# Performance work log

Measured on AMD Instinct MI355X. Metric: run time of the kernel, lower is better.

The kernel has to match this reference:

```python
import jax, jax.numpy as jnp
import numpy as np

B, T, F_IN, F_OUT = 16, 2048, 128, 128
ALPHA = 0.2  # LeakyReLU negative slope
MASK_VAL = -1e9


def setup_inputs() -> dict:
    key = jax.random.key(0)
    kx, kw, ka, kadj = jax.random.split(key, 4)
    # xavier_uniform-ish scale for W and a (gain=1.414)
    w_bound = 1.414 * np.sqrt(6.0 / (F_IN + F_OUT))
    a_bound = 1.414 * np.sqrt(6.0 / (2 * F_OUT + 1))
    x = jax.random.normal(kx, (B, T, F_IN), jnp.float32)
    W = jax.random.uniform(kw, (F_IN, F_OUT), jnp.float32, -w_bound, w_bound)
    a = jax.random.uniform(ka, (2 * F_OUT, 1), jnp.float32, -a_bound, a_bound)
    adj = jax.random.randint(kadj, (B, T, T), 0, 2, jnp.int32)
    return {"x": x, "adj": adj, "W": W, "a": a}


def reference(x, adj, W, a):
    # h: [B,T,F_OUT]
    h = jnp.einsum('btf,fo->bto', x, W)
    # Additive GAT score decomposition: e[b,i,j] = leakyrelu(h_i . a1 + h_j . a2)
    # Mathematically identical to cat([h_i,h_j]) @ a, without the BxTxTx2F tensor.
    a1 = a[:F_OUT, 0]   # [F_OUT]
    a2 = a[F_OUT:, 0]   # [F_OUT]
    s1 = h @ a1         # [B,T]
    s2 = h @ a2         # [B,T]
    e = jax.nn.leaky_relu(s1[:, :, None] + s2[:, None, :], ALPHA)  # [B,T,T]
    e = jnp.where(adj == 0, MASK_VAL, e)
    att = jax.nn.softmax(e, axis=-1)  # [B,T,T]
    # dropout=0.0 / eval mode -> identity
    return att @ h  # [B,T,F_OUT]
```

## Files before the change

### kernel.cpp

```cpp
#include <hip/hip_runtime.h>
#include <hip/hip_bf16.h>

#define TT 2048
#define NB 16
#define FD 128
#define ALPHA 0.2f

typedef __attribute__((ext_vector_type(8))) short short8;
typedef __attribute__((ext_vector_type(4))) float f32x4;
typedef __attribute__((ext_vector_type(16))) float f32x16;

static __device__ __forceinline__ unsigned short f2bf(float f) {
    unsigned u = __float_as_uint(f);
    u += 0x7FFF + ((u >> 16) & 1);
    return (unsigned short)(u >> 16);
}
static __device__ __forceinline__ unsigned short bfbits(float f) {
    return __builtin_bit_cast(unsigned short, __float2bfloat16(f));
}

__global__ __launch_bounds__(256) void k_pack(const int* __restrict__ adj,
                                              unsigned char* __restrict__ bm)
{
    const int tid = threadIdx.x;
    const int w = tid >> 6, l = tid & 63;
    const int row = blockIdx.x * 4 + w;
    const int* ap = adj + (size_t)row * TT + l * 4;
    unsigned char* op = bm + (size_t)row * 256;

    #pragma unroll
    for (int rd = 0; rd < 8; ++rd) {
        int4 q = *reinterpret_cast<const int4*>(ap + rd * 256);
        unsigned n =  min((unsigned)q.x, 1u)
                   | (min((unsigned)q.y, 1u) << 1)
                   | (min((unsigned)q.z, 1u) << 2)
                   | (min((unsigned)q.w, 1u) << 3);
        unsigned pn = (unsigned)__shfl_xor((int)n, 1);
        if ((l & 1) == 0)
            op[rd * 32 + (l >> 1)] = (unsigned char)(n | (pn << 4));
    }
}

__global__ __launch_bounds__(256) void k_wt(const float* __restrict__ W,
                                            unsigned short* __restrict__ WT)
{
    int fid = blockIdx.x * 256 + threadIdx.x;
    int k = fid >> 5;
    int f = (fid & 31) << 2;
    float4 w4 = *reinterpret_cast<const float4*>(W + k * FD + f);
    WT[(f + 0) * FD + k] = f2bf(w4.x);
    WT[(f + 1) * FD + k] = f2bf(w4.y);
    WT[(f + 2) * FD + k] = f2bf(w4.z);
    WT[(f + 3) * FD + k] = f2bf(w4.w);
}

__global__ __launch_bounds__(256) void k_h(const float* __restrict__ x,
                                           const unsigned short* __restrict__ WT,
                                           const float* __restrict__ a,
                                           unsigned short* __restrict__ hF,
                                           float* __restrict__ s1,
                                           float* __restrict__ s2)
{
    __shared__ unsigned short hs[128][72];

    const int tid = threadIdx.x;
    const int b  = blockIdx.x >> 5;
    const int t0 = (blockIdx.x & 31) << 6;
    const int w = tid >> 6, l = tid & 63, g = l >> 4, r15 = l & 15;

    const float* xrow = x + ((size_t)(b * TT + t0 + w * 16 + r15)) * FD;

    f32x4 acc[8] = {};

    #pragma unroll
    for (int m = 0; m < 4; ++m) {
        const int koff = m * 32 + g * 8;
        float4 xa = *reinterpret_cast<const float4*>(xrow + koff);
        float4 xb = *reinterpret_cast<const float4*>(xrow + koff + 4);
        short8 af;
        af[0] = (short)f2bf(xa.x); af[1] = (short)f2bf(xa.y);
        af[2] = (short)f2bf(xa.z); af[3] = (short)f2bf(xa.w);
        af[4] = (short)f2bf(xb.x); af[5] = (short)f2bf(xb.y);
        af[6] = (short)f2bf(xb.z); af[7] = (short)f2bf(xb.w);
        #pragma unroll
        for (int n = 0; n < 8; ++n) {
            short8 bfr = *reinterpret_cast<const short8*>(WT + (n * 16 + r15) * FD + koff);
            acc[n] = __builtin_amdgcn_mfma_f32_16x16x32_bf16(af, bfr, acc[n], 0, 0, 0);
        }
    }

    float p1[4] = {0.f, 0.f, 0.f, 0.f}, p2[4] = {0.f, 0.f, 0.f, 0.f};
    #pragma unroll
    for (int n = 0; n < 8; ++n) {
        float a1v = a[n * 16 + r15];
        float a2v = a[FD + n * 16 + r15];
        #pragma unroll
        for (int r = 0; r < 4; ++r) {
            p1[r] += acc[n][r] * a1v;
            p2[r] += acc[n][r] * a2v;
        }
    }
    #pragma unroll
    for (int r = 0; r < 4; ++r) {
        #pragma unroll
        for (int off = 8; off >= 1; off >>= 1) {
            p1[r] += __shfl_xor(p1[r], off);
            p2[r] += __shfl_xor(p2[r], off);
        }
    }
    if (r15 == 0) {
        const int trow = t0 + w * 16 + g * 4;
        #pragma unroll
        for (int r = 0; r < 4; ++r) {
            s1[b * TT + trow + r] = p1[r];
            s2[b * TT + trow + r] = p2[r];
        }
    }

    #pragma unroll
    for (int n = 0; n < 8; ++n)
        #pragma unroll
        for (int r = 0; r < 4; ++r)
            hs[n * 16 + r15][w * 16 + g * 4 + r] = f2bf(acc[n][r]);
    __syncthreads();

    #pragma unroll
    for (int it = 0; it < 4; ++it) {
        int idx = it * 256 + tid;
        int lp = idx & 63;
        int frag = idx >> 6;
        int n32 = frag & 3, tl = frag >> 2;
        int fsrc = n32 * 32 + (lp & 31);
        int tsrc = tl * 16 + (lp >> 5) * 8;
        short8 v = *reinterpret_cast<const short8*>(&hs[fsrc][tsrc]);
        *reinterpret_cast<short8*>(
            hF + (((size_t)(b * 128 + (t0 >> 4) + tl)) * 4 + n32) * 512 + lp * 8) = v;
    }
}

__global__ __launch_bounds__(256, 4) void k_att(const unsigned char* __restrict__ bm,
                                                const unsigned short* __restrict__ hF,
                                                const float* __restrict__ s1,
                                                const float* __restrict__ s2,
                                                float* __restrict__ out)
{
    __shared__ __align__(16) float red[2][32][132];
    __shared__ float dsum[4][32];

    const int tid = threadIdx.x;
    const int wg = (blockIdx.x & 7) * 128 + (blockIdx.x >> 3);
    const int b  = wg >> 6;
    const int i0 = (wg & 63) << 5;
    const int w = tid >> 6, l = tid & 63;
    const int il = l & 31, h = l >> 5;
    const int hsh = h * 8;

    const int jbeg = w * (TT / 4);
    const float s1v = s1[b * TT + i0 + il];
    const float* s2p = s2 + b * TT + jbeg + h * 8;
    const unsigned char* bmrow = bm + ((size_t)(b * TT + i0 + il)) * 256 + w * 64;
    const unsigned short* hfp = hF + ((size_t)(b * 128 + (jbeg >> 4))) * 4 * 512 + l * 8;

    f32x16 acc[4] = {};
    float rsum = 0.f;

    short8 bb[2][4];
    #pragma unroll
    for (int n = 0; n < 4; ++n)
        bb[0][n] = *reinterpret_cast<const short8*>(hfp + (size_t)n * 512);

    uint4 bq;

    #pragma unroll
    for (int t = 0; t < 32; ++t) {
        const int cur = t & 1;
        if (t < 31) {
            #pragma unroll
            for (int n = 0; n < 4; ++n)
                bb[cur ^ 1][n] = *reinterpret_cast<const short8*>(
                    hfp + (size_t)((t + 1) * 4 + n) * 512);
        }
        if ((t & 7) == 0)
            bq = *reinterpret_cast<const uint4*>(bmrow + (t >> 3) * 16);
        const int wi = (t & 7) >> 1;
        const unsigned wsel = wi == 0 ? bq.x : wi == 1 ? bq.y : wi == 2 ? bq.z : bq.w;
        const unsigned bits = (wsel >> ((t & 1) * 16 + hsh)) & 0xffu;

        float4 sa = *reinterpret_cast<const float4*>(s2p + t * 16);
        float4 sb = *reinterpret_cast<const float4*>(s2p + t * 16 + 4);
        float csf[8] = {sa.x, sa.y, sa.z, sa.w, sb.x, sb.y, sb.z, sb.w};
        float pv[8];
        #pragma unroll
        for (int e = 0; e < 8; ++e) {
            float s = s1v + csf[e];
            s = fmaxf(s, ALPHA * s);
            float p = ((int)(bits << (31 - e)) < 0) ? __expf(s) : 0.f;
            rsum += p;
            pv[e] = p;
        }
        short8 af;
        #pragma unroll
        for (int e = 0; e < 8; ++e)
            af[e] = (short)bfbits(pv[e]);
        #pragma unroll
        for (int n = 0; n < 4; ++n)
            acc[n] = __builtin_amdgcn_mfma_f32_32x32x16_bf16(af, bb[cur][n], acc[n], 0, 0, 0);
    }

    rsum += __shfl_xor(rsum, 32);
    if (l < 32) dsum[w][l] = rsum;

    if (w < 2) {
        #pragma unroll
        for (int n = 0; n < 4; ++n)
            #pragma unroll
            for (int r = 0; r < 16; ++r) {
                int irow = (r & 3) + 8 * (r >> 2) + 4 * h;
                red[w][irow][n * 32 + il] = acc[n][r];
            }
    }
    __syncthreads();
    if (w >= 2) {
        #pragma unroll
        for (int n = 0; n < 4; ++n)
            #pragma unroll
            for (int r = 0; r < 16; ++r) {
                int irow = (r & 3) + 8 * (r >> 2) + 4 * h;
                red[w - 2][irow][n * 32 + il] += acc[n][r];
            }
    }
    __syncthreads();

    #pragma unroll
    for (int it = 0; it < 4; ++it) {
        int e = it * 256 + tid;
        int row = e >> 5;
        int c4 = (e & 31) << 2;
        float4 v0 = *reinterpret_cast<const float4*>(&red[0][row][c4]);
        float4 v1 = *reinterpret_cast<const float4*>(&red[1][row][c4]);
        float dn = dsum[0][row] + dsum[1][row] + dsum[2][row] + dsum[3][row];
        float ri = 1.0f / dn;
        float4 o;
        o.x = (v0.x + v1.x) * ri;
        o.y = (v0.y + v1.y) * ri;
        o.z = (v0.z + v1.z) * ri;
        o.w = (v0.w + v1.w) * ri;
        *reinterpret_cast<float4*>(out + ((size_t)(b * TT + i0 + row)) * FD + c4) = o;
    }
}

extern "C" void kernel_launch(void* const* d_in, const int* in_sizes, int n_in,
                              void* d_out, int out_size, void* d_ws, size_t ws_size,
                              hipStream_t stream)
{
    const float* x  = (const float*)d_in[0];
    const int* adj  = (const int*)d_in[1];
    const float* W  = (const float*)d_in[2];
    const float* a  = (const float*)d_in[3];
    float* out = (float*)d_out;

    unsigned short* hF = (unsigned short*)d_ws;
    float* s1 = (float*)((char*)d_ws + (size_t)NB * FD * TT * 2);
    float* s2 = s1 + NB * TT;
    unsigned short* WT = (unsigned short*)(s2 + NB * TT);
    unsigned char* bm = (unsigned char*)(WT + FD * FD);

    k_wt  <<<16, 256, 0, stream>>>(W, WT);
    k_h   <<<NB * (TT / 64), 256, 0, stream>>>(x, WT, a, hF, s1, s2);
    k_pack<<<NB * TT / 4, 256, 0, stream>>>(adj, bm);
    k_att <<<NB * (TT / 32), 256, 0, stream>>>(bm, hF, s1, s2, out);
}
```

Baseline: 106.6 us.

## Deepen hF prefetch, stage s2 in LDS, preload mask, split k_h across 8 waves

The attention kernel now prefetches two steps of hF fragments with a triple buffer, copies the per-batch s2 row into shared memory once, and loads all of its adjacency mask bytes up front. Its occupancy hint drops from 4 to 3 blocks per SM to leave room for the extra registers. The projection kernel runs 512 threads, splitting the output features across wave pairs and combining the partial s1/s2 sums through shared memory. The intent is to hide global memory latency in the main loop, at the cost of more register and LDS pressure and lower occupancy.

```diff
diff --git a/kernel.cpp b/kernel.cpp
--- a/kernel.cpp
+++ b/kernel.cpp
@@ -54,7 +54,7 @@
     WT[(f + 3) * FD + k] = f2bf(w4.w);
 }
 
-__global__ __launch_bounds__(256) void k_h(const float* __restrict__ x,
+__global__ __launch_bounds__(512) void k_h(const float* __restrict__ x,
                                            const unsigned short* __restrict__ WT,
                                            const float* __restrict__ a,
                                            unsigned short* __restrict__ hF,
@@ -62,15 +62,17 @@
                                            float* __restrict__ s2)
 {
     __shared__ unsigned short hs[128][72];
+    __shared__ float ps1[2][64], ps2[2][64];
 
     const int tid = threadIdx.x;
     const int b  = blockIdx.x >> 5;
     const int t0 = (blockIdx.x & 31) << 6;
-    const int w = tid >> 6, l = tid & 63, g = l >> 4, r15 = l & 15;
-
-    const float* xrow = x + ((size_t)(b * TT + t0 + w * 16 + r15)) * FD;
-
-    f32x4 acc[8] = {};
+    const int wv = tid >> 6, l = tid & 63, g = l >> 4, r15 = l & 15;
+    const int wr = wv >> 1, ng = wv & 1;
+
+    const float* xrow = x + ((size_t)(b * TT + t0 + wr * 16 + r15)) * FD;
+
+    f32x4 acc[4] = {};
 
     #pragma unroll
     for (int m = 0; m < 4; ++m) {
@@ -83,21 +85,23 @@
         af[4] = (short)f2bf(xb.x); af[5] = (short)f2bf(xb.y);
         af[6] = (short)f2bf(xb.z); af[7] = (short)f2bf(xb.w);
         #pragma unroll
-        for (int n = 0; n < 8; ++n) {
+        for (int nn = 0; nn < 4; ++nn) {
+            const int n = ng * 4 + nn;
             short8 bfr = *reinterpret_cast<const short8*>(WT + (n * 16 + r15) * FD + koff);
-            acc[n] = __builtin_amdgcn_mfma_f32_16x16x32_bf16(af, bfr, acc[n], 0, 0, 0);
+            acc[nn] = __builtin_amdgcn_mfma_f32_16x16x32_bf16(af, bfr, acc[nn], 0, 0, 0);
         }
     }
 
     float p1[4] = {0.f, 0.f, 0.f, 0.f}, p2[4] = {0.f, 0.f, 0.f, 0.f};
     #pragma unroll
-    for (int n = 0; n < 8; ++n) {
+    for (int nn = 0; nn < 4; ++nn) {
+        const int n = ng * 4 + nn;
         float a1v = a[n * 16 + r15];
         float a2v = a[FD + n * 16 + r15];
         #pragma unroll
         for (int r = 0; r < 4; ++r) {
-            p1[r] += acc[n][r] * a1v;
-            p2[r] += acc[n][r] * a2v;
+            p1[r] += acc[nn][r] * a1v;
+            p2[r] += acc[nn][r] * a2v;
         }
     }
     #pragma unroll
@@ -109,24 +113,28 @@
         }
     }
     if (r15 == 0) {
-        const int trow = t0 + w * 16 + g * 4;
         #pragma unroll
         for (int r = 0; r < 4; ++r) {
-            s1[b * TT + trow + r] = p1[r];
-            s2[b * TT + trow + r] = p2[r];
-        }
-    }
-
-    #pragma unroll
-    for (int n = 0; n < 8; ++n)
+            ps1[ng][wr * 16 + g * 4 + r] = p1[r];
+            ps2[ng][wr * 16 + g * 4 + r] = p2[r];
+        }
+    }
+
+    #pragma unroll
+    for (int nn = 0; nn < 4; ++nn)
         #pragma unroll
         for (int r = 0; r < 4; ++r)
-            hs[n * 16 + r15][w * 16 + g * 4 + r] = f2bf(acc[n][r]);
-    __syncthreads();
-
-    #pragma unroll
-    for (int it = 0; it < 4; ++it) {
-        int idx = it * 256 + tid;
+            hs[(ng * 4 + nn) * 16 + r15][wr * 16 + g * 4 + r] = f2bf(acc[nn][r]);
+    __syncthreads();
+
+    if (tid < 64) {
+        s1[b * TT + t0 + tid] = ps1[0][tid] + ps1[1][tid];
+        s2[b * TT + t0 + tid] = ps2[0][tid] + ps2[1][tid];
+    }
+
+    #pragma unroll
+    for (int it = 0; it < 2; ++it) {
+        int idx = it * 512 + tid;
         int lp = idx & 63;
         int frag = idx >> 6;
         int n32 = frag & 3, tl = frag >> 2;
@@ -138,12 +146,13 @@
     }
 }
 
-__global__ __launch_bounds__(256, 4) void k_att(const unsigned char* __restrict__ bm,
+__global__ __launch_bounds__(256, 3) void k_att(const unsigned char* __restrict__ bm,
                                                 const unsigned short* __restrict__ hF,
                                                 const float* __restrict__ s1,
                                                 const float* __restrict__ s2,
                                                 float* __restrict__ out)
 {
+    __shared__ float s2b[TT];
     __shared__ __align__(16) float red[2][32][132];
     __shared__ float dsum[4][32];
 
@@ -155,39 +164,55 @@
     const int il = l & 31, h = l >> 5;
     const int hsh = h * 8;
 
+    {
+        float4 v0 = *reinterpret_cast<const float4*>(s2 + b * TT + tid * 8);
+        float4 v1 = *reinterpret_cast<const float4*>(s2 + b * TT + tid * 8 + 4);
+        *reinterpret_cast<float4*>(&s2b[tid * 8])     = v0;
+        *reinterpret_cast<float4*>(&s2b[tid * 8 + 4]) = v1;
+    }
+    const float s1v = s1[b * TT + i0 + il];
+
     const int jbeg = w * (TT / 4);
-    const float s1v = s1[b * TT + i0 + il];
-    const float* s2p = s2 + b * TT + jbeg + h * 8;
     const unsigned char* bmrow = bm + ((size_t)(b * TT + i0 + il)) * 256 + w * 64;
     const unsigned short* hfp = hF + ((size_t)(b * 128 + (jbeg >> 4))) * 4 * 512 + l * 8;
 
+    uint4 bq[4];
+    bq[0] = *reinterpret_cast<const uint4*>(bmrow);
+    bq[1] = *reinterpret_cast<const uint4*>(bmrow + 16);
+    bq[2] = *reinterpret_cast<const uint4*>(bmrow + 32);
+    bq[3] = *reinterpret_cast<const uint4*>(bmrow + 48);
+
+    __syncthreads();
+    const float* s2w = &s2b[jbeg + h * 8];
+
     f32x16 acc[4] = {};
     float rsum = 0.f;
 
-    short8 bb[2][4];
-    #pragma unroll
-    for (int n = 0; n < 4; ++n)
-        bb[0][n] = *reinterpret_cast<const short8*>(hfp + (size_t)n * 512);
-
-    uint4 bq;
+    short8 bb[3][4];
+    #pragma unroll
+    for (int p = 0; p < 2; ++p)
+        #pragma unroll
+        for (int n = 0; n < 4; ++n)
+            bb[p][n] = *reinterpret_cast<const short8*>(hfp + (size_t)(p * 4 + n) * 512);
 
     #pragma unroll
     for (int t = 0; t < 32; ++t) {
-        const int cur = t & 1;
-        if (t < 31) {
+        const int slot = t % 3;
+        if (t < 30) {
+            const int ns = (t + 2) % 3;
             #pragma unroll
             for (int n = 0; n < 4; ++n)
-                bb[cur ^ 1][n] = *reinterpret_cast<const short8*>(
-                    hfp + (size_t)((t + 1) * 4 + n) * 512);
-        }
-        if ((t & 7) == 0)
-            bq = *reinterpret_cast<const uint4*>(bmrow + (t >> 3) * 16);
-        const int wi = (t & 7) >> 1;
-        const unsigned wsel = wi == 0 ? bq.x : wi == 1 ? bq.y : wi == 2 ? bq.z : bq.w;
+                bb[ns][n] = *reinterpret_cast<const short8*>(
+                    hfp + (size_t)((t + 2) * 4 + n) * 512);
+        }
+        const int wi = t >> 3;
+        const uint4 bqw = bq[wi];
+        const int ci = (t >> 1) & 3;
+        const unsigned wsel = ci == 0 ? bqw.x : ci == 1 ? bqw.y : ci == 2 ? bqw.z : bqw.w;
         const unsigned bits = (wsel >> ((t & 1) * 16 + hsh)) & 0xffu;
 
-        float4 sa = *reinterpret_cast<const float4*>(s2p + t * 16);
-        float4 sb = *reinterpret_cast<const float4*>(s2p + t * 16 + 4);
+        float4 sa = *reinterpret_cast<const float4*>(&s2w[t * 16]);
+        float4 sb = *reinterpret_cast<const float4*>(&s2w[t * 16 + 4]);
         float csf[8] = {sa.x, sa.y, sa.z, sa.w, sb.x, sb.y, sb.z, sb.w};
         float pv[8];
         #pragma unroll
@@ -204,7 +229,8 @@
             af[e] = (short)bfbits(pv[e]);
         #pragma unroll
         for (int n = 0; n < 4; ++n)
-            acc[n] = __builtin_amdgcn_mfma_f32_32x32x16_bf16(af, bb[cur][n], acc[n], 0, 0, 0);
+            acc[n] = __builtin_amdgcn_mfma_f32_32x32x16_bf16(af, bb[slot][n],
+                                                             acc[n], 0, 0, 0);
     }
 
     rsum += __shfl_xor(rsum, 32);
@@ -266,7 +292,7 @@
     unsigned char* bm = (unsigned char*)(WT + FD * FD);
 
     k_wt  <<<16, 256, 0, stream>>>(W, WT);
-    k_h   <<<NB * (TT / 64), 256, 0, stream>>>(x, WT, a, hF, s1, s2);
+    k_h   <<<NB * (TT / 64), 512, 0, stream>>>(x, WT, a, hF, s1, s2);
     k_pack<<<NB * TT / 4, 256, 0, stream>>>(adj, bm);
     k_att <<<NB * (TT / 32), 256, 0, stream>>>(bm, hF, s1, s2, out);
 }
```

New measurement: 108.3 us. Within noise of the previous version (+1.6%).
